# Optimization experiments

Hardware: AMD Instinct MI355X
Metric: run time of the kernel (lower is better)

## Reference

```python
import math
import jax, jax.numpy as jnp
import numpy as np

H_HEADS = 8
K_MAX = 64
MIN_WINDOW = 1.0
SHARPNESS = 5.0


def rmsnorm(x, w, eps=1e-6):
    x32 = x.astype(jnp.float32)
    var = jnp.mean(x32 * x32, axis=-1, keepdims=True)
    return (w * (x32 * jax.lax.rsqrt(var + eps))).astype(x.dtype)


def setup_inputs() -> dict:
    key = jax.random.key(0)
    ks = jax.random.split(key, 12)
    B, L, C = 1, 4096, 256
    H, K = H_HEADS, K_MAX
    s = 0.02
    return {
        "x": jax.random.normal(ks[0], (B, L, C), jnp.float32),
        "window_w": jax.random.normal(ks[1], (C, H), jnp.float32) * s,
        "window_b": jnp.zeros((H,), jnp.float32),
        "window_gamma": jnp.ones((H,), jnp.float32),
        "offset_w": jax.random.normal(ks[2], (C, H), jnp.float32) * s,
        "offset_b": jnp.zeros((H,), jnp.float32),
        "offset_gamma": jnp.ones((H,), jnp.float32),
        "kernel_w": jax.random.normal(ks[3], (C, H * K), jnp.float32) * s,
        "kernel_b": jnp.zeros((H * K,), jnp.float32),
        "kernel_gamma": jnp.ones((H * K,), jnp.float32),
        "v_w": jax.random.normal(ks[4], (C, C), jnp.float32) * (1.0 / math.sqrt(C)),
        "v_b": jnp.zeros((C,), jnp.float32),
        "out_w": jax.random.normal(ks[5], (C, C), jnp.float32) * s,
    }


def reference(x, window_w, window_b, window_gamma, offset_w, offset_b, offset_gamma,
              kernel_w, kernel_b, kernel_gamma, v_w, v_b, out_w):
    B, L, C = x.shape
    H, K = H_HEADS, K_MAX
    D = C // H
    max_window = min(int(math.sqrt(L)), K)
    half = max_window // 2
    max_offset = int(math.sqrt(L))
    N = 2 * half + 1  # num_offsets

    # per-position learned window sizes, center offsets, kernel weights
    window_raw = jax.nn.sigmoid(rmsnorm(x @ window_w + window_b, window_gamma))
    window_sizes = MIN_WINDOW + window_raw * (max_window - MIN_WINDOW)      # [B,L,H]
    center_offsets = jnp.tanh(rmsnorm(x @ offset_w + offset_b, offset_gamma)) * max_offset  # [B,L,H]
    kernel_weights = jax.nn.silu(rmsnorm(x @ kernel_w + kernel_b, kernel_gamma)).reshape(B, L, H, K)
    v = (x @ v_w + v_b).reshape(B, L, H, D)

    local = jnp.arange(-half, half + 1, dtype=x.dtype)                      # [N]
    positions = jnp.arange(L, dtype=x.dtype).reshape(1, L, 1, 1)
    neighbor = positions + center_offsets[..., None] + local.reshape(1, 1, 1, N)  # [B,L,H,N]
    valid = (neighbor >= 0) & (neighbor < L)
    nclamp = jnp.clip(neighbor, 0, L - 1)

    rel = jnp.abs(local).reshape(1, 1, 1, N) / (window_sizes[..., None] / 2 + 1e-6)
    window_mask = jax.nn.sigmoid(SHARPNESS * (1.0 - rel)) * valid.astype(x.dtype)

    # kernel interpolation by relative distance
    kidx = jnp.clip(rel, 0, 1) * (K - 1)
    i_fl = jnp.clip(kidx.astype(jnp.int32), 0, K - 2)                       # [B,L,H,N]
    i_ce = i_fl + 1
    w_ce = kidx - i_fl.astype(x.dtype)
    k_fl = jnp.take_along_axis(kernel_weights, i_fl, axis=-1)
    k_ce = jnp.take_along_axis(kernel_weights, i_ce, axis=-1)
    kernel_interp = k_fl * (1.0 - w_ce) + k_ce * w_ce

    attn = kernel_interp * window_mask
    attn = attn / (jnp.sum(attn, axis=-1, keepdims=True) + 1e-6)            # [B,L,H,N]

    # bilinear gather of values at fractional neighbor positions
    p_fl = jnp.clip(jnp.floor(nclamp).astype(jnp.int32), 0, L - 1)
    p_ce = jnp.clip(p_fl + 1, 0, L - 1)
    frac = nclamp - p_fl.astype(x.dtype)                                    # [B,L,H,N]

    v_bh = v.transpose(0, 2, 1, 3)                                          # [B,H,L,D]
    idx_f = p_fl.transpose(0, 2, 1, 3).reshape(B, H, L * N)
    idx_c = p_ce.transpose(0, 2, 1, 3).reshape(B, H, L * N)
    v_fl = jnp.take_along_axis(v_bh, idx_f[..., None], axis=2).reshape(B, H, L, N, D)
    v_ce = jnp.take_along_axis(v_bh, idx_c[..., None], axis=2).reshape(B, H, L, N, D)
    frac_bh = frac.transpose(0, 2, 1, 3)[..., None]                         # [B,H,L,N,1]
    v_nb = v_fl * (1.0 - frac_bh) + v_ce * frac_bh                          # [B,H,L,N,D]

    attn_bh = attn.transpose(0, 2, 1, 3)                                    # [B,H,L,N]
    out = jnp.einsum('bhln,bhlnd->bhld', attn_bh, v_nb)                     # [B,H,L,D]
    out = out.transpose(0, 2, 1, 3).reshape(B, L, C)
    return jax.nn.silu(out @ out_w)
```

## Files before the change

### kernel.cpp

```cpp
#include <hip/hip_runtime.h>
#include <math.h>

#define L_SEQ 4096
#define C_DIM 256
#define H_HEADS 8
#define K_MAX 64
#define D_HEAD 32
#define HALF_W 32
#define N_OFF 65
#define HK 512

__device__ __forceinline__ float sigmoidf_(float x) { return 1.0f / (1.0f + expf(-x)); }

__global__ void proj_gemm(const float* __restrict__ A, const float* __restrict__ kw_w,
                          const float* __restrict__ vw, const float* __restrict__ kb,
                          const float* __restrict__ vb,
                          float* __restrict__ kwbuf, float* __restrict__ vbuf) {
    __shared__ float As[16][68];
    __shared__ float Bs[16][68];

    const int tid = threadIdx.x;
    const int tx = tid & 15;
    const int ty = tid >> 4;
    const int l0 = blockIdx.y * 64;
    const int n0 = blockIdx.x * 64;

    const int am = tid >> 2;
    const int ak = (tid & 3) * 4;
    const int bk = tid >> 4;
    const int bn = (tid & 15) * 4;

    const float* Bsrc;
    int ldb, coff;
    if (n0 < 512) { Bsrc = kw_w; ldb = 512; coff = n0; }
    else          { Bsrc = vw;   ldb = 256; coff = n0 - 512; }

    float acc[4][4];
#pragma unroll
    for (int i = 0; i < 4; ++i)
#pragma unroll
        for (int jj = 0; jj < 4; ++jj) acc[i][jj] = 0.0f;

    float4 av = *(const float4*)&A[(l0 + am) * C_DIM + ak];
    float4 bv = *(const float4*)&Bsrc[bk * ldb + coff + bn];

    for (int k0 = 0; k0 < C_DIM; k0 += 16) {
        __syncthreads();
        As[ak + 0][am] = av.x;
        As[ak + 1][am] = av.y;
        As[ak + 2][am] = av.z;
        As[ak + 3][am] = av.w;
        *(float4*)&Bs[bk][bn] = bv;
        __syncthreads();
        if (k0 + 16 < C_DIM) {
            av = *(const float4*)&A[(l0 + am) * C_DIM + (k0 + 16) + ak];
            bv = *(const float4*)&Bsrc[(k0 + 16 + bk) * ldb + coff + bn];
        }
#pragma unroll
        for (int kk = 0; kk < 16; ++kk) {
            const float4 a4 = *(const float4*)&As[kk][ty * 4];
            const float4 b4 = *(const float4*)&Bs[kk][tx * 4];
            const float ar[4] = {a4.x, a4.y, a4.z, a4.w};
            const float br[4] = {b4.x, b4.y, b4.z, b4.w};
#pragma unroll
            for (int i = 0; i < 4; ++i)
#pragma unroll
                for (int jj = 0; jj < 4; ++jj)
                    acc[i][jj] = fmaf(ar[i], br[jj], acc[i][jj]);
        }
    }

    const int g0 = n0 + tx * 4;
    float4 bz;
    float* dst;
    int stride, col;
    if (g0 < 512) { bz = *(const float4*)&kb[g0];       dst = kwbuf; stride = 512; col = g0; }
    else          { bz = *(const float4*)&vb[g0 - 512]; dst = vbuf;  stride = 256; col = g0 - 512; }
#pragma unroll
    for (int i = 0; i < 4; ++i) {
        const int row = l0 + ty * 4 + i;
        float4 o;
        o.x = acc[i][0] + bz.x;
        o.y = acc[i][1] + bz.y;
        o.z = acc[i][2] + bz.z;
        o.w = acc[i][3] + bz.w;
        *(float4*)&dst[row * stride + col] = o;
    }
}

__global__ void conv_fused(const float* __restrict__ x,
                           const float* __restrict__ ww, const float* __restrict__ wb,
                           const float* __restrict__ wg,
                           const float* __restrict__ ow, const float* __restrict__ ob,
                           const float* __restrict__ og,
                           const float* __restrict__ kg,
                           const float* __restrict__ kwraw, const float* __restrict__ v,
                           float* __restrict__ out) {
    const int l = blockIdx.x;
    const int tid = threadIdx.x;

    __shared__ float red[256];
    __shared__ float rs_s;
    __shared__ float kwrow[HK];
    __shared__ float wsz[H_HEADS], ofs[H_HEADS];
    __shared__ float attn[H_HEADS][N_OFF];
    __shared__ int   pfl[H_HEADS][N_OFF];
    __shared__ float frac[H_HEADS][N_OFF];
    __shared__ float inv_denom[H_HEADS];

    {
        const int j = tid;
        const float* row = kwraw + l * HK;
        const float z0 = row[j];
        const float z1 = row[j + 256];
        red[j] = z0 * z0 + z1 * z1;
        __syncthreads();
        for (int s = 128; s > 0; s >>= 1) {
            if (j < s) red[j] += red[j + s];
            __syncthreads();
        }
        if (j == 0) rs_s = rsqrtf(red[0] / (float)HK + 1e-6f);
        __syncthreads();
        const float rs = rs_s;
        const float n0v = kg[j] * z0 * rs;
        const float n1v = kg[j + 256] * z1 * rs;
        kwrow[j]       = n0v * sigmoidf_(n0v);
        kwrow[j + 256] = n1v * sigmoidf_(n1v);
    }

    if (tid < 64) {
        const int lane = tid;
        const float* xr = x + l * C_DIM;
        float accw[H_HEADS], acco[H_HEADS];
#pragma unroll
        for (int h = 0; h < H_HEADS; ++h) { accw[h] = 0.0f; acco[h] = 0.0f; }
#pragma unroll
        for (int i = 0; i < C_DIM / 64; ++i) {
            const int c = lane + i * 64;
            const float xv = xr[c];
            const float* wwc = ww + c * H_HEADS;
            const float* owc = ow + c * H_HEADS;
#pragma unroll
            for (int h = 0; h < H_HEADS; ++h) {
                accw[h] = fmaf(xv, wwc[h], accw[h]);
                acco[h] = fmaf(xv, owc[h], acco[h]);
            }
        }
#pragma unroll
        for (int off = 32; off > 0; off >>= 1) {
#pragma unroll
            for (int h = 0; h < H_HEADS; ++h) {
                accw[h] += __shfl_xor(accw[h], off);
                acco[h] += __shfl_xor(acco[h], off);
            }
        }
        if (lane == 0) {
            float zw[H_HEADS], zo[H_HEADS];
            float ssw = 0.0f, sso = 0.0f;
#pragma unroll
            for (int h = 0; h < H_HEADS; ++h) {
                zw[h] = accw[h] + wb[h];
                zo[h] = acco[h] + ob[h];
                ssw += zw[h] * zw[h];
                sso += zo[h] * zo[h];
            }
            const float rw = rsqrtf(ssw / (float)H_HEADS + 1e-6f);
            const float ro = rsqrtf(sso / (float)H_HEADS + 1e-6f);
#pragma unroll
            for (int h = 0; h < H_HEADS; ++h) {
                const float nw = wg[h] * zw[h] * rw;
                const float no = og[h] * zo[h] * ro;
                wsz[h] = 1.0f + sigmoidf_(nw) * 63.0f;
                ofs[h] = tanhf(no) * 64.0f;
            }
        }
    }
    __syncthreads();

    for (int t = tid; t < H_HEADS * N_OFF; t += 256) {
        const int h = t / N_OFF;
        const int n = t - h * N_OFF;
        const float ws  = wsz[h];
        const float off = ofs[h];
        const float local = (float)(n - HALF_W);
        const float neighbor = (float)l + off + local;
        const bool valid = (neighbor >= 0.0f) && (neighbor < (float)L_SEQ);
        const float nc = fminf(fmaxf(neighbor, 0.0f), (float)(L_SEQ - 1));

        const float rel = fabsf(local) / (ws * 0.5f + 1e-6f);
        const float mask = sigmoidf_(5.0f * (1.0f - rel)) * (valid ? 1.0f : 0.0f);

        const float kidx = fminf(rel, 1.0f) * (float)(K_MAX - 1);
        int ifl = (int)kidx;
        ifl = min(ifl, K_MAX - 2);
        const float wce = kidx - (float)ifl;
        const float kf = kwrow[h * K_MAX + ifl];
        const float kc = kwrow[h * K_MAX + ifl + 1];
        attn[h][n] = (kf * (1.0f - wce) + kc * wce) * mask;

        int p = (int)floorf(nc);
        p = min(max(p, 0), L_SEQ - 1);
        pfl[h][n] = p;
        frac[h][n] = nc - (float)p;
    }
    __syncthreads();

    if (tid < H_HEADS) {
        float s = 0.0f;
        for (int n = 0; n < N_OFF; ++n) s += attn[tid][n];
        inv_denom[tid] = 1.0f / (s + 1e-6f);
    }
    __syncthreads();

    const int h = tid >> 5;
    const int d = tid & 31;
    float acc = 0.0f;
    for (int n = 0; n < N_OFF; ++n) {
        const float a = attn[h][n];
        const int   p = pfl[h][n];
        const float f = frac[h][n];
        const int  pc = min(p + 1, L_SEQ - 1);
        const float vf = v[p * C_DIM + h * D_HEAD + d];
        const float vc = v[pc * C_DIM + h * D_HEAD + d];
        acc = fmaf(a, vf + f * (vc - vf), acc);
    }
    out[l * C_DIM + h * D_HEAD + d] = acc * inv_denom[h];
}

__global__ void out_gemm(const float* __restrict__ A, const float* __restrict__ W,
                         float* __restrict__ out) {
    __shared__ float As[16][36];
    __shared__ float Bs[16][68];

    const int tid = threadIdx.x;
    const int tx = tid & 15;
    const int ty = tid >> 4;
    const int l0 = blockIdx.y * 32;
    const int n0 = blockIdx.x * 64;

    const int bk = tid >> 4;
    const int bn = (tid & 15) * 4;
    const int am = (tid & 127) >> 2;
    const int ak = (tid & 3) * 4;
    const bool aload = tid < 128;

    float acc[2][4];
#pragma unroll
    for (int i = 0; i < 2; ++i)
#pragma unroll
        for (int jj = 0; jj < 4; ++jj) acc[i][jj] = 0.0f;

    float4 av, bv;
    if (aload) av = *(const float4*)&A[(l0 + am) * C_DIM + ak];
    bv = *(const float4*)&W[bk * C_DIM + n0 + bn];

    for (int k0 = 0; k0 < C_DIM; k0 += 16) {
        __syncthreads();
        if (aload) {
            As[ak + 0][am] = av.x;
            As[ak + 1][am] = av.y;
            As[ak + 2][am] = av.z;
            As[ak + 3][am] = av.w;
        }
        *(float4*)&Bs[bk][bn] = bv;
        __syncthreads();
        if (k0 + 16 < C_DIM) {
            if (aload) av = *(const float4*)&A[(l0 + am) * C_DIM + (k0 + 16) + ak];
            bv = *(const float4*)&W[(k0 + 16 + bk) * C_DIM + n0 + bn];
        }
#pragma unroll
        for (int kk = 0; kk < 16; ++kk) {
            const float a0 = As[kk][ty * 2 + 0];
            const float a1 = As[kk][ty * 2 + 1];
            const float4 b4 = *(const float4*)&Bs[kk][tx * 4];
            const float br[4] = {b4.x, b4.y, b4.z, b4.w};
#pragma unroll
            for (int jj = 0; jj < 4; ++jj) {
                acc[0][jj] = fmaf(a0, br[jj], acc[0][jj]);
                acc[1][jj] = fmaf(a1, br[jj], acc[1][jj]);
            }
        }
    }

    const int g0 = n0 + tx * 4;
#pragma unroll
    for (int i = 0; i < 2; ++i) {
        const int row = l0 + ty * 2 + i;
        float4 o;
        o.x = acc[i][0] * sigmoidf_(acc[i][0]);
        o.y = acc[i][1] * sigmoidf_(acc[i][1]);
        o.z = acc[i][2] * sigmoidf_(acc[i][2]);
        o.w = acc[i][3] * sigmoidf_(acc[i][3]);
        *(float4*)&out[row * C_DIM + g0] = o;
    }
}

extern "C" void kernel_launch(void* const* d_in, const int* in_sizes, int n_in,
                              void* d_out, int out_size, void* d_ws, size_t ws_size,
                              hipStream_t stream) {
    const float* x    = (const float*)d_in[0];
    const float* ww   = (const float*)d_in[1];
    const float* wb   = (const float*)d_in[2];
    const float* wg   = (const float*)d_in[3];
    const float* ow   = (const float*)d_in[4];
    const float* ob   = (const float*)d_in[5];
    const float* og   = (const float*)d_in[6];
    const float* kw_w = (const float*)d_in[7];
    const float* kb   = (const float*)d_in[8];
    const float* kg   = (const float*)d_in[9];
    const float* vw   = (const float*)d_in[10];
    const float* vb   = (const float*)d_in[11];
    const float* outw = (const float*)d_in[12];
    float* y = (float*)d_out;

    float* ws_f    = (float*)d_ws;
    float* kwbuf   = ws_f;
    float* vbuf    = kwbuf + L_SEQ * HK;
    float* convbuf = vbuf + L_SEQ * C_DIM;

    proj_gemm<<<dim3(12, L_SEQ / 64), 256, 0, stream>>>(x, kw_w, vw, kb, vb, kwbuf, vbuf);
    conv_fused<<<L_SEQ, 256, 0, stream>>>(x, ww, wb, wg, ow, ob, og, kg, kwbuf, vbuf, convbuf);
    out_gemm<<<dim3(C_DIM / 64, L_SEQ / 32), 256, 0, stream>>>(convbuf, outw, y);
}
```

Baseline: 163.8 us.

## Enlarge projection GEMM row tile and pack conv tap metadata into float4

The projection GEMM now computes 128 rows per block with an 8x4 register tile per thread instead of 64 rows and 4x4, halving the grid along L and doubling reuse of each B tile. In the fused conv kernel, the per-tap attention weight, fraction and precomputed floor/ceil value offsets are packed into one float4 shared array, so each tap needs one LDS read and no index arithmetic in the gather loop, which is also partially unrolled. The per-head window/offset finalisation is spread across 8 lanes instead of one. The bigger GEMM tile raises register use and halves block count (384 blocks), which may lower occupancy.

```diff
diff --git a/kernel.cpp b/kernel.cpp
--- a/kernel.cpp
+++ b/kernel.cpp
@@ -16,17 +16,18 @@
                           const float* __restrict__ vw, const float* __restrict__ kb,
                           const float* __restrict__ vb,
                           float* __restrict__ kwbuf, float* __restrict__ vbuf) {
-    __shared__ float As[16][68];
+    __shared__ float As[16][132];
     __shared__ float Bs[16][68];
 
     const int tid = threadIdx.x;
     const int tx = tid & 15;
     const int ty = tid >> 4;
-    const int l0 = blockIdx.y * 64;
+    const int l0 = blockIdx.y * 128;
     const int n0 = blockIdx.x * 64;
 
-    const int am = tid >> 2;
-    const int ak = (tid & 3) * 4;
+    const int ar0 = tid >> 2;
+    const int ac0 = (tid & 3) * 4;
+    const int ar1 = ar0 + 64;
     const int bk = tid >> 4;
     const int bn = (tid & 15) * 4;
 
@@ -35,35 +36,43 @@
     if (n0 < 512) { Bsrc = kw_w; ldb = 512; coff = n0; }
     else          { Bsrc = vw;   ldb = 256; coff = n0 - 512; }
 
-    float acc[4][4];
-#pragma unroll
-    for (int i = 0; i < 4; ++i)
+    float acc[8][4];
+#pragma unroll
+    for (int i = 0; i < 8; ++i)
 #pragma unroll
         for (int jj = 0; jj < 4; ++jj) acc[i][jj] = 0.0f;
 
-    float4 av = *(const float4*)&A[(l0 + am) * C_DIM + ak];
-    float4 bv = *(const float4*)&Bsrc[bk * ldb + coff + bn];
+    float4 av0 = *(const float4*)&A[(l0 + ar0) * C_DIM + ac0];
+    float4 av1 = *(const float4*)&A[(l0 + ar1) * C_DIM + ac0];
+    float4 bv  = *(const float4*)&Bsrc[bk * ldb + coff + bn];
 
     for (int k0 = 0; k0 < C_DIM; k0 += 16) {
         __syncthreads();
-        As[ak + 0][am] = av.x;
-        As[ak + 1][am] = av.y;
-        As[ak + 2][am] = av.z;
-        As[ak + 3][am] = av.w;
+        As[ac0 + 0][ar0] = av0.x;
+        As[ac0 + 1][ar0] = av0.y;
+        As[ac0 + 2][ar0] = av0.z;
+        As[ac0 + 3][ar0] = av0.w;
+        As[ac0 + 0][ar1] = av1.x;
+        As[ac0 + 1][ar1] = av1.y;
+        As[ac0 + 2][ar1] = av1.z;
+        As[ac0 + 3][ar1] = av1.w;
         *(float4*)&Bs[bk][bn] = bv;
         __syncthreads();
         if (k0 + 16 < C_DIM) {
-            av = *(const float4*)&A[(l0 + am) * C_DIM + (k0 + 16) + ak];
-            bv = *(const float4*)&Bsrc[(k0 + 16 + bk) * ldb + coff + bn];
+            av0 = *(const float4*)&A[(l0 + ar0) * C_DIM + (k0 + 16) + ac0];
+            av1 = *(const float4*)&A[(l0 + ar1) * C_DIM + (k0 + 16) + ac0];
+            bv  = *(const float4*)&Bsrc[(k0 + 16 + bk) * ldb + coff + bn];
         }
 #pragma unroll
         for (int kk = 0; kk < 16; ++kk) {
-            const float4 a4 = *(const float4*)&As[kk][ty * 4];
-            const float4 b4 = *(const float4*)&Bs[kk][tx * 4];
-            const float ar[4] = {a4.x, a4.y, a4.z, a4.w};
+            const float4 a4lo = *(const float4*)&As[kk][ty * 8];
+            const float4 a4hi = *(const float4*)&As[kk][ty * 8 + 4];
+            const float4 b4   = *(const float4*)&Bs[kk][tx * 4];
+            const float ar[8] = {a4lo.x, a4lo.y, a4lo.z, a4lo.w,
+                                 a4hi.x, a4hi.y, a4hi.z, a4hi.w};
             const float br[4] = {b4.x, b4.y, b4.z, b4.w};
 #pragma unroll
-            for (int i = 0; i < 4; ++i)
+            for (int i = 0; i < 8; ++i)
 #pragma unroll
                 for (int jj = 0; jj < 4; ++jj)
                     acc[i][jj] = fmaf(ar[i], br[jj], acc[i][jj]);
@@ -77,8 +86,8 @@
     if (g0 < 512) { bz = *(const float4*)&kb[g0];       dst = kwbuf; stride = 512; col = g0; }
     else          { bz = *(const float4*)&vb[g0 - 512]; dst = vbuf;  stride = 256; col = g0 - 512; }
 #pragma unroll
-    for (int i = 0; i < 4; ++i) {
-        const int row = l0 + ty * 4 + i;
+    for (int i = 0; i < 8; ++i) {
+        const int row = l0 + ty * 8 + i;
         float4 o;
         o.x = acc[i][0] + bz.x;
         o.y = acc[i][1] + bz.y;
@@ -103,9 +112,7 @@
     __shared__ float rs_s;
     __shared__ float kwrow[HK];
     __shared__ float wsz[H_HEADS], ofs[H_HEADS];
-    __shared__ float attn[H_HEADS][N_OFF];
-    __shared__ int   pfl[H_HEADS][N_OFF];
-    __shared__ float frac[H_HEADS][N_OFF];
+    __shared__ float4 tap[H_HEADS][N_OFF];
     __shared__ float inv_denom[H_HEADS];
 
     {
@@ -154,7 +161,7 @@
                 acco[h] += __shfl_xor(acco[h], off);
             }
         }
-        if (lane == 0) {
+        if (lane < H_HEADS) {
             float zw[H_HEADS], zo[H_HEADS];
             float ssw = 0.0f, sso = 0.0f;
 #pragma unroll
@@ -166,13 +173,10 @@
             }
             const float rw = rsqrtf(ssw / (float)H_HEADS + 1e-6f);
             const float ro = rsqrtf(sso / (float)H_HEADS + 1e-6f);
-#pragma unroll
-            for (int h = 0; h < H_HEADS; ++h) {
-                const float nw = wg[h] * zw[h] * rw;
-                const float no = og[h] * zo[h] * ro;
-                wsz[h] = 1.0f + sigmoidf_(nw) * 63.0f;
-                ofs[h] = tanhf(no) * 64.0f;
-            }
+            const float nw = wg[lane] * zw[lane] * rw;
+            const float no = og[lane] * zo[lane] * ro;
+            wsz[lane] = 1.0f + sigmoidf_(nw) * 63.0f;
+            ofs[lane] = tanhf(no) * 64.0f;
         }
     }
     __syncthreads();
@@ -196,18 +200,25 @@
         const float wce = kidx - (float)ifl;
         const float kf = kwrow[h * K_MAX + ifl];
         const float kc = kwrow[h * K_MAX + ifl + 1];
-        attn[h][n] = (kf * (1.0f - wce) + kc * wce) * mask;
+        const float attnv = (kf * (1.0f - wce) + kc * wce) * mask;
 
         int p = (int)floorf(nc);
         p = min(max(p, 0), L_SEQ - 1);
-        pfl[h][n] = p;
-        frac[h][n] = nc - (float)p;
+        const int pc = min(p + 1, L_SEQ - 1);
+        const float fr = nc - (float)p;
+
+        float4 tv;
+        tv.x = attnv;
+        tv.y = fr;
+        tv.z = __int_as_float(p * C_DIM + h * D_HEAD);
+        tv.w = __int_as_float(pc * C_DIM + h * D_HEAD);
+        tap[h][n] = tv;
     }
     __syncthreads();
 
     if (tid < H_HEADS) {
         float s = 0.0f;
-        for (int n = 0; n < N_OFF; ++n) s += attn[tid][n];
+        for (int n = 0; n < N_OFF; ++n) s += tap[tid][n].x;
         inv_denom[tid] = 1.0f / (s + 1e-6f);
     }
     __syncthreads();
@@ -215,14 +226,14 @@
     const int h = tid >> 5;
     const int d = tid & 31;
     float acc = 0.0f;
+#pragma unroll 5
     for (int n = 0; n < N_OFF; ++n) {
-        const float a = attn[h][n];
-        const int   p = pfl[h][n];
-        const float f = frac[h][n];
-        const int  pc = min(p + 1, L_SEQ - 1);
-        const float vf = v[p * C_DIM + h * D_HEAD + d];
-        const float vc = v[pc * C_DIM + h * D_HEAD + d];
-        acc = fmaf(a, vf + f * (vc - vf), acc);
+        const float4 t = tap[h][n];
+        const int bf = __float_as_int(t.z);
+        const int bc = __float_as_int(t.w);
+        const float vf = v[bf + d];
+        const float vc = v[bc + d];
+        acc = fmaf(t.x, fmaf(t.y, vc - vf, vf), acc);
     }
     out[l * C_DIM + h * D_HEAD + d] = acc * inv_denom[h];
 }
@@ -318,7 +329,7 @@
     float* vbuf    = kwbuf + L_SEQ * HK;
     float* convbuf = vbuf + L_SEQ * C_DIM;
 
-    proj_gemm<<<dim3(12, L_SEQ / 64), 256, 0, stream>>>(x, kw_w, vw, kb, vb, kwbuf, vbuf);
+    proj_gemm<<<dim3(12, L_SEQ / 128), 256, 0, stream>>>(x, kw_w, vw, kb, vb, kwbuf, vbuf);
     conv_fused<<<L_SEQ, 256, 0, stream>>>(x, ww, wb, wg, ow, ob, og, kg, kwbuf, vbuf, convbuf);
     out_gemm<<<dim3(C_DIM / 64, L_SEQ / 32), 256, 0, stream>>>(convbuf, outw, y);
 }
```

Result: faster. 154.2 us (-5.8%).
